# Optimization experiments

Hardware: AMD Instinct MI355X
Metric: run time of the kernel (lower is better)

## Reference

```python
import jax, jax.numpy as jnp
import numpy as np

DIM = 1024
NHEAD = 16
HEAD_DIM = DIM // NHEAD


def setup_inputs() -> dict:
    key = jax.random.key(0)
    k_x, k_wqkv, k_bqkv, k_wp, k_bp = jax.random.split(key, 5)
    scale = 1.0 / np.sqrt(DIM)
    return {
        "x": jax.random.normal(k_x, (4, 2048, DIM), dtype=jnp.float32),
        "w_qkv": jax.random.uniform(k_wqkv, (DIM, 3 * DIM), minval=-scale, maxval=scale, dtype=jnp.float32),
        "b_qkv": jax.random.uniform(k_bqkv, (3 * DIM,), minval=-scale, maxval=scale, dtype=jnp.float32),
        "w_proj": jax.random.uniform(k_wp, (DIM, DIM), minval=-scale, maxval=scale, dtype=jnp.float32),
        "b_proj": jax.random.uniform(k_bp, (DIM,), minval=-scale, maxval=scale, dtype=jnp.float32),
    }


def reference(x, w_qkv, b_qkv, w_proj, b_proj):
    B, N, D = x.shape
    # qkv projection: [B,N,3D] -> [3,B,H,N,hd]
    qkv = x @ w_qkv + b_qkv
    qkv = qkv.reshape(B, N, 3, NHEAD, HEAD_DIM).transpose(2, 0, 3, 1, 4)
    q, k, v = qkv[0], qkv[1], qkv[2]
    # naive full attention: scores [B,H,N,N]
    attn = jnp.einsum("bhqd,bhkd->bhqk", q, k) / jnp.sqrt(jnp.float32(HEAD_DIM))
    attn = jax.nn.softmax(attn, axis=-1)
    out = jnp.einsum("bhqk,bhkd->bhqd", attn, v)  # [B,H,N,hd]
    out = out.transpose(0, 2, 1, 3).reshape(B, N, D)
    return out @ w_proj + b_proj
```

## Files before the change

kernel.cpp:

```cpp
#include <hip/hip_runtime.h>
#include <math.h>

#define DIM     1024
#define NHEAD   16
#define HD      64
#define BATCH   4
#define SEQ     2048
#define MTOT    (BATCH * SEQ)
#define QKV_N   (3 * DIM)

typedef __attribute__((ext_vector_type(8))) short bf16x8;
typedef __attribute__((ext_vector_type(4))) float f32x4;
typedef unsigned int u32;
typedef unsigned short u16;

__device__ __forceinline__ u16 f2bf(float f) {
    u32 u = __float_as_uint(f);
    return (u16)((u + 0x7fffu + ((u >> 16) & 1u)) >> 16);
}

__device__ __forceinline__ float exp2_fast(float x) {
    float r; asm("v_exp_f32 %0, %1" : "=v"(r) : "v"(x)); return r;
}

__device__ __forceinline__ u32 cvtpk_bf16(float lo, float hi) {
    u32 r; asm("v_cvt_pk_bf16_f32 %0, %1, %2" : "=v"(r) : "v"(lo), "v"(hi));
    return r;
}

__device__ __forceinline__ void gload_lds16(const u16* g, u16* l) {
    __builtin_amdgcn_global_load_lds((const __attribute__((address_space(1))) u32*)g,
                                     (__attribute__((address_space(3))) u32*)l, 16, 0, 0);
}

__global__ __launch_bounds__(256) void cast_x(const float* __restrict__ in,
                                              u16* __restrict__ out) {
    const int i = (blockIdx.x * 256 + threadIdx.x) * 4;
    const float4 v = *(const float4*)&in[i];
    ushort4 o;
    o.x = f2bf(v.x); o.y = f2bf(v.y); o.z = f2bf(v.z); o.w = f2bf(v.w);
    *(ushort4*)&out[i] = o;
}

__global__ __launch_bounds__(256) void cast_transpose(const float* __restrict__ W,
                                                      u16* __restrict__ Wt,
                                                      int K, int N) {
    __shared__ float Ls[64][65];
    const int k0 = blockIdx.x * 64, n0 = blockIdx.y * 64;
    const int t = threadIdx.x;
    const int r = t >> 4, c4 = (t & 15) << 2;
    #pragma unroll
    for (int i = 0; i < 4; ++i) {
        const float4 v = *(const float4*)&W[(size_t)(k0 + r + i * 16) * N + n0 + c4];
        Ls[r + i * 16][c4 + 0] = v.x; Ls[r + i * 16][c4 + 1] = v.y;
        Ls[r + i * 16][c4 + 2] = v.z; Ls[r + i * 16][c4 + 3] = v.w;
    }
    __syncthreads();
    #pragma unroll
    for (int i = 0; i < 4; ++i) {
        const int nr = r + i * 16;
        ushort4 o;
        o.x = f2bf(Ls[c4 + 0][nr]); o.y = f2bf(Ls[c4 + 1][nr]);
        o.z = f2bf(Ls[c4 + 2][nr]); o.w = f2bf(Ls[c4 + 3][nr]);
        *(ushort4*)&Wt[(size_t)(n0 + nr) * K + k0 + c4] = o;
    }
}

#define GEMM_STAGE(buf, kof, Aptr, Bptr)                                       \
    _Pragma("unroll") for (int i = 0; i < 2; ++i) {                            \
        const int row = w * 32 + i * 16 + (lane >> 2);                         \
        const int slot = (lane & 3) ^ ((row >> 1) & 3);                        \
        gload_lds16(&Aptr[(size_t)(m0 + row) * DIM + (kof) + slot * 8],        \
                    &As[buf][(w * 32 + i * 16) * 32]);                         \
        gload_lds16(&Bptr[(size_t)(n0 + row) * DIM + (kof) + slot * 8],        \
                    &Bs[buf][(w * 32 + i * 16) * 32]);                         \
    }

#define GEMM_MAINLOOP(Aptr, Bptr)                                              \
    __shared__ __align__(16) u16 As[2][128 * 32];                              \
    __shared__ __align__(16) u16 Bs[2][128 * 32];                              \
    const int t = threadIdx.x;                                                 \
    const int lane = t & 63, w = t >> 6;                                       \
    const int n0 = blockIdx.x * 128;                                           \
    const int m0 = blockIdx.y * 128;                                           \
    const int wm = (w & 1) * 64, wn = (w >> 1) * 64;                           \
    const int g = lane >> 4, li = lane & 15;                                   \
    f32x4 acc[4][4];                                                           \
    _Pragma("unroll") for (int mt = 0; mt < 4; ++mt)                           \
        _Pragma("unroll") for (int nt = 0; nt < 4; ++nt)                       \
            acc[mt][nt] = (f32x4){0.f, 0.f, 0.f, 0.f};                         \
    GEMM_STAGE(0, 0, Aptr, Bptr)                                               \
    __syncthreads();                                                           \
    int cur = 0;                                                               \
    for (int k0 = 0; k0 < DIM; k0 += 32) {                                     \
        if (k0 + 32 < DIM) { GEMM_STAGE(cur ^ 1, k0 + 32, Aptr, Bptr) }        \
        bf16x8 a[4], b[4];                                                     \
        _Pragma("unroll") for (int mt = 0; mt < 4; ++mt) {                     \
            const int row = wm + mt * 16 + li;                                 \
            const int slot = g ^ ((row >> 1) & 3);                             \
            a[mt] = *(const bf16x8*)&As[cur][row * 32 + slot * 8];             \
        }                                                                      \
        _Pragma("unroll") for (int nt = 0; nt < 4; ++nt) {                     \
            const int row = wn + nt * 16 + li;                                 \
            const int slot = g ^ ((row >> 1) & 3);                             \
            b[nt] = *(const bf16x8*)&Bs[cur][row * 32 + slot * 8];             \
        }                                                                      \
        _Pragma("unroll") for (int mt = 0; mt < 4; ++mt)                       \
            _Pragma("unroll") for (int nt = 0; nt < 4; ++nt)                   \
                acc[mt][nt] = __builtin_amdgcn_mfma_f32_16x16x32_bf16(         \
                    a[mt], b[nt], acc[mt][nt], 0, 0, 0);                       \
        __syncthreads();                                                       \
        cur ^= 1;                                                              \
    }

#define QSCALE 0.18033688011112042f
__global__ __launch_bounds__(256) void gemm_qkv(
    const u16* __restrict__ A, const u16* __restrict__ Bt,
    const float* __restrict__ bias,
    u16* __restrict__ qo, u16* __restrict__ ko, u16* __restrict__ vo)
{
    GEMM_MAINLOOP(A, Bt)
    #pragma unroll
    for (int nt = 0; nt < 4; ++nt) {
        const int n = n0 + wn + nt * 16 + li;
        const int which = n >> 10;
        const int head  = (n >> 6) & 15;
        const int hd    = n & 63;
        const float bv = bias[n];
        if (which == 2) {
            #pragma unroll
            for (int mt = 0; mt < 4; ++mt) {
                const int m = m0 + wm + mt * 16 + g * 4;
                const int bb = m >> 11, tok = m & 2047;
                const u32 p0 = cvtpk_bf16(acc[mt][nt][0] + bv, acc[mt][nt][1] + bv);
                const u32 p1 = cvtpk_bf16(acc[mt][nt][2] + bv, acc[mt][nt][3] + bv);
                u16* d = &vo[((size_t)(bb * NHEAD + head) * HD + hd) * SEQ + tok];
                *(u32*)&d[0] = p0;
                *(u32*)&d[2] = p1;
            }
        } else {
            u16* dst = (which == 0) ? qo : ko;
            const float scale = (which == 0) ? QSCALE : 1.0f;
            #pragma unroll
            for (int mt = 0; mt < 4; ++mt) {
                #pragma unroll
                for (int r = 0; r < 4; ++r) {
                    const int m = m0 + wm + mt * 16 + g * 4 + r;
                    const int bb = m >> 11, tok = m & 2047;
                    dst[((size_t)(bb * NHEAD + head) * SEQ + tok) * HD + hd] =
                        f2bf((acc[mt][nt][r] + bv) * scale);
                }
            }
        }
    }
}

__global__ __launch_bounds__(256) void gemm_proj(
    const u16* __restrict__ A, const u16* __restrict__ Bt,
    const float* __restrict__ bias, float* __restrict__ out)
{
    GEMM_MAINLOOP(A, Bt)
    #pragma unroll
    for (int nt = 0; nt < 4; ++nt) {
        const int n = n0 + wn + nt * 16 + li;
        const float bv = bias[n];
        #pragma unroll
        for (int mt = 0; mt < 4; ++mt) {
            #pragma unroll
            for (int r = 0; r < 4; ++r) {
                const int m = m0 + wm + mt * 16 + g * 4 + r;
                out[(size_t)m * DIM + n] = acc[mt][nt][r] + bv;
            }
        }
    }
}

#define NKT  (SEQ / 64)
#define ATTN_STAGE(buf, ktile)                                                 \
    _Pragma("unroll") for (int i = 0; i < 2; ++i) {                            \
        const int rho = w * 16 + i * 8 + srow;                                 \
        const int key = (rho & 32) | (((rho >> 2) & 3) << 3)                   \
                      | (((rho >> 4) & 1) << 2) | (rho & 3);                   \
        const int sl = (sslot ^ (rho & 7)) << 3;                               \
        gload_lds16(&kg[(size_t)(ktile) * (64 * HD) + (size_t)key * HD + sl],  \
                    &Ks[buf][(w * 16 + i * 8) * 64]);                          \
        gload_lds16(&vg[(size_t)rho * SEQ + (ktile) * 64 + sl],                \
                    &Vs[buf][(w * 16 + i * 8) * 64]);                          \
    }

__global__ __launch_bounds__(256) void attn_mfma(
    const u16* __restrict__ q, const u16* __restrict__ k,
    const u16* __restrict__ v, u16* __restrict__ ao)
{
    __shared__ __align__(16) u16 Ks[3][64 * 64];
    __shared__ __align__(16) u16 Vs[3][64 * 64];

    const int t = threadIdx.x;
    const int lane = t & 63, w = t >> 6;
    const int g = lane >> 4, li = lane & 15;

    int flat = blockIdx.y * 16 + blockIdx.x;
    flat = (flat & 7) * 128 + (flat >> 3);
    const int q0 = (flat & 15) * 128;
    const int bh = flat >> 4;
    const size_t base = (size_t)bh * SEQ * HD;
    const u16* kg = k + base;
    const u16* vg = v + (size_t)bh * HD * SEQ;

    bf16x8 qf[2][2];
    #pragma unroll
    for (int h = 0; h < 2; ++h) {
        const size_t qrow = base + (size_t)(q0 + w * 32 + h * 16 + li) * HD;
        qf[h][0] = *(const bf16x8*)&q[qrow + g * 8];
        qf[h][1] = *(const bf16x8*)&q[qrow + 32 + g * 8];
    }

    float lsum[2] = {0.f, 0.f};
    f32x4 oacc[2][4];
    #pragma unroll
    for (int h = 0; h < 2; ++h)
        #pragma unroll
        for (int nt = 0; nt < 4; ++nt) oacc[h][nt] = (f32x4){0.f, 0.f, 0.f, 0.f};

    const int srow = lane >> 3;
    const int sslot = lane & 7;
    const int x8 = li & 15 & 7;

    ATTN_STAGE(0, 0)
    ATTN_STAGE(1, 1)

    int c0 = 0;
    for (int kt = 0; kt < NKT; ++kt) {
        if (kt + 1 < NKT) {
            asm volatile("s_waitcnt vmcnt(4)" ::: "memory");
        } else {
            asm volatile("s_waitcnt vmcnt(0)" ::: "memory");
        }
        __builtin_amdgcn_s_barrier();
        __builtin_amdgcn_sched_barrier(0);

        if (kt + 2 < NKT) {
            const int sslot3 = (c0 >= 1) ? c0 - 1 : c0 + 2;
            ATTN_STAGE(sslot3, kt + 2)
        }

        const u16* Kc = Ks[c0];
        const u16* Vc = Vs[c0];

        f32x4 s[2][4];
        #pragma unroll
        for (int nt = 0; nt < 4; ++nt) {
            const int rowb = (nt * 16 + li) << 6;
            const bf16x8 kf0 = *(const bf16x8*)&Kc[rowb + ((g ^ x8) << 3)];
            const bf16x8 kf1 = *(const bf16x8*)&Kc[rowb + (((g ^ 4) ^ x8) << 3)];
            #pragma unroll
            for (int h = 0; h < 2; ++h) {
                f32x4 c = (f32x4){0.f, 0.f, 0.f, 0.f};
                c = __builtin_amdgcn_mfma_f32_16x16x32_bf16(kf0, qf[h][0], c, 0, 0, 0);
                c = __builtin_amdgcn_mfma_f32_16x16x32_bf16(kf1, qf[h][1], c, 0, 0, 0);
                s[h][nt] = c;
            }
        }

        bf16x8 pb[2][2];
        #pragma unroll
        for (int h = 0; h < 2; ++h) {
            float rs = 0.f;
            #pragma unroll
            for (int nt = 0; nt < 4; ++nt)
                #pragma unroll
                for (int r = 0; r < 4; ++r) {
                    const float p = exp2_fast(s[h][nt][r]);
                    s[h][nt][r] = p;
                    rs += p;
                }
            lsum[h] += rs;
            #pragma unroll
            for (int ks = 0; ks < 2; ++ks) {
                union { u32 u[4]; bf16x8 v8; } uu;
                uu.u[0] = cvtpk_bf16(s[h][2 * ks][0],     s[h][2 * ks][1]);
                uu.u[1] = cvtpk_bf16(s[h][2 * ks][2],     s[h][2 * ks][3]);
                uu.u[2] = cvtpk_bf16(s[h][2 * ks + 1][0], s[h][2 * ks + 1][1]);
                uu.u[3] = cvtpk_bf16(s[h][2 * ks + 1][2], s[h][2 * ks + 1][3]);
                pb[h][ks] = uu.v8;
            }
        }

        #pragma unroll
        for (int ks = 0; ks < 2; ++ks) {
            #pragma unroll
            for (int nt = 0; nt < 4; ++nt) {
                const bf16x8 vb = *(const bf16x8*)
                    &Vc[((nt * 16 + li) << 6) + (((g ^ (ks << 2)) ^ x8) << 3)];
                #pragma unroll
                for (int h = 0; h < 2; ++h)
                    oacc[h][nt] = __builtin_amdgcn_mfma_f32_16x16x32_bf16(
                        vb, pb[h][ks], oacc[h][nt], 0, 0, 0);
            }
        }

        c0 = (c0 == 2) ? 0 : c0 + 1;
    }

    const int bb = bh >> 4, hh = bh & 15;
    #pragma unroll
    for (int h = 0; h < 2; ++h) {
        float lf = lsum[h];
        lf += __shfl_xor(lf, 16);
        lf += __shfl_xor(lf, 32);
        const float inv = 1.0f / lf;
        const int tok = q0 + w * 32 + h * 16 + li;
        u16* dst = &ao[(size_t)(bb * SEQ + tok) * DIM + hh * HD];
        #pragma unroll
        for (int nt = 0; nt < 4; ++nt) {
            const u32 p0 = cvtpk_bf16(oacc[h][nt][0] * inv, oacc[h][nt][1] * inv);
            const u32 p1 = cvtpk_bf16(oacc[h][nt][2] * inv, oacc[h][nt][3] * inv);
            *(u32*)&dst[nt * 16 + g * 4]     = p0;
            *(u32*)&dst[nt * 16 + g * 4 + 2] = p1;
        }
    }
}

extern "C" void kernel_launch(void* const* d_in, const int* in_sizes, int n_in,
                              void* d_out, int out_size, void* d_ws, size_t ws_size,
                              hipStream_t stream)
{
    const float* x      = (const float*)d_in[0];
    const float* w_qkv  = (const float*)d_in[1];
    const float* b_qkv  = (const float*)d_in[2];
    const float* w_proj = (const float*)d_in[3];
    const float* b_proj = (const float*)d_in[4];
    float* out = (float*)d_out;

    u16* xb  = (u16*)d_ws;
    u16* wqt = xb  + (size_t)MTOT * DIM;
    u16* wpt = wqt + (size_t)QKV_N * DIM;
    u16* qb  = wpt + (size_t)DIM * DIM;
    u16* kb  = qb  + (size_t)MTOT * DIM;
    u16* vb  = kb  + (size_t)MTOT * DIM;
    u16* aob = vb  + (size_t)MTOT * DIM;

    cast_x<<<(MTOT * DIM) / 1024, 256, 0, stream>>>(x, xb);
    cast_transpose<<<dim3(DIM / 64, QKV_N / 64), 256, 0, stream>>>(w_qkv, wqt, DIM, QKV_N);
    cast_transpose<<<dim3(DIM / 64, DIM / 64), 256, 0, stream>>>(w_proj, wpt, DIM, DIM);

    gemm_qkv<<<dim3(QKV_N / 128, MTOT / 128), 256, 0, stream>>>(xb, wqt, b_qkv, qb, kb, vb);
    attn_mfma<<<dim3(SEQ / 128, BATCH * NHEAD), 256, 0, stream>>>(qb, kb, vb, aob);
    gemm_proj<<<dim3(DIM / 128, MTOT / 128), 256, 0, stream>>>(aob, wpt, b_proj, out);
}
```

Measured before the change: 210.3 us.

## Split attention warps across key halves and reduce partial outputs via LDS

Changes the per-warp work split in the attention kernel. Each warp now owns 64 query rows and half of each 64-key tile (2x2 warp grid) instead of 32 query rows over the full key tile. Each warp reuses its K fragments across 4 query subtiles, and V/P MFMAs drop to one k-step per tile. Partial O accumulators and row sums from the two key-half warps are combined through LDS at the end. The cost is more accumulator registers (16 f32x4 versus 8), possibly lower occupancy, and an extra LDS reduction with two block barriers.

```diff
diff --git a/kernel.cpp b/kernel.cpp
--- a/kernel.cpp
+++ b/kernel.cpp
@@ -198,6 +198,7 @@
     const int t = threadIdx.x;
     const int lane = t & 63, w = t >> 6;
     const int g = lane >> 4, li = lane & 15;
+    const int qw = w & 1, kw = w >> 1;
 
     int flat = blockIdx.y * 16 + blockIdx.x;
     flat = (flat & 7) * 128 + (flat >> 3);
@@ -207,24 +208,24 @@
     const u16* kg = k + base;
     const u16* vg = v + (size_t)bh * HD * SEQ;
 
-    bf16x8 qf[2][2];
-    #pragma unroll
-    for (int h = 0; h < 2; ++h) {
-        const size_t qrow = base + (size_t)(q0 + w * 32 + h * 16 + li) * HD;
+    bf16x8 qf[4][2];
+    #pragma unroll
+    for (int h = 0; h < 4; ++h) {
+        const size_t qrow = base + (size_t)(q0 + qw * 64 + h * 16 + li) * HD;
         qf[h][0] = *(const bf16x8*)&q[qrow + g * 8];
         qf[h][1] = *(const bf16x8*)&q[qrow + 32 + g * 8];
     }
 
-    float lsum[2] = {0.f, 0.f};
-    f32x4 oacc[2][4];
-    #pragma unroll
-    for (int h = 0; h < 2; ++h)
+    float lsum[4] = {0.f, 0.f, 0.f, 0.f};
+    f32x4 oacc[4][4];
+    #pragma unroll
+    for (int h = 0; h < 4; ++h)
         #pragma unroll
         for (int nt = 0; nt < 4; ++nt) oacc[h][nt] = (f32x4){0.f, 0.f, 0.f, 0.f};
 
     const int srow = lane >> 3;
     const int sslot = lane & 7;
-    const int x8 = li & 15 & 7;
+    const int x8 = li & 7;
 
     ATTN_STAGE(0, 0)
     ATTN_STAGE(1, 1)
@@ -240,83 +241,103 @@
         __builtin_amdgcn_sched_barrier(0);
 
         if (kt + 2 < NKT) {
-            const int sslot3 = (c0 >= 1) ? c0 - 1 : c0 + 2;
-            ATTN_STAGE(sslot3, kt + 2)
+            const int st3 = (c0 >= 1) ? c0 - 1 : c0 + 2;
+            ATTN_STAGE(st3, kt + 2)
         }
 
         const u16* Kc = Ks[c0];
         const u16* Vc = Vs[c0];
 
-        f32x4 s[2][4];
-        #pragma unroll
-        for (int nt = 0; nt < 4; ++nt) {
-            const int rowb = (nt * 16 + li) << 6;
-            const bf16x8 kf0 = *(const bf16x8*)&Kc[rowb + ((g ^ x8) << 3)];
-            const bf16x8 kf1 = *(const bf16x8*)&Kc[rowb + (((g ^ 4) ^ x8) << 3)];
-            #pragma unroll
-            for (int h = 0; h < 2; ++h) {
+        bf16x8 kf[2][2];
+        #pragma unroll
+        for (int ntl = 0; ntl < 2; ++ntl) {
+            const int rowb = ((kw * 2 + ntl) * 16 + li) << 6;
+            kf[ntl][0] = *(const bf16x8*)&Kc[rowb + ((g ^ x8) << 3)];
+            kf[ntl][1] = *(const bf16x8*)&Kc[rowb + (((g ^ 4) ^ x8) << 3)];
+        }
+
+        bf16x8 pb[4];
+        #pragma unroll
+        for (int h = 0; h < 4; ++h) {
+            f32x4 s[2];
+            #pragma unroll
+            for (int ntl = 0; ntl < 2; ++ntl) {
                 f32x4 c = (f32x4){0.f, 0.f, 0.f, 0.f};
-                c = __builtin_amdgcn_mfma_f32_16x16x32_bf16(kf0, qf[h][0], c, 0, 0, 0);
-                c = __builtin_amdgcn_mfma_f32_16x16x32_bf16(kf1, qf[h][1], c, 0, 0, 0);
-                s[h][nt] = c;
-            }
-        }
-
-        bf16x8 pb[2][2];
-        #pragma unroll
-        for (int h = 0; h < 2; ++h) {
+                c = __builtin_amdgcn_mfma_f32_16x16x32_bf16(kf[ntl][0], qf[h][0], c, 0, 0, 0);
+                c = __builtin_amdgcn_mfma_f32_16x16x32_bf16(kf[ntl][1], qf[h][1], c, 0, 0, 0);
+                s[ntl] = c;
+            }
             float rs = 0.f;
             #pragma unroll
-            for (int nt = 0; nt < 4; ++nt)
+            for (int ntl = 0; ntl < 2; ++ntl)
                 #pragma unroll
                 for (int r = 0; r < 4; ++r) {
-                    const float p = exp2_fast(s[h][nt][r]);
-                    s[h][nt][r] = p;
+                    const float p = exp2_fast(s[ntl][r]);
+                    s[ntl] [r] = p;
                     rs += p;
                 }
             lsum[h] += rs;
-            #pragma unroll
-            for (int ks = 0; ks < 2; ++ks) {
-                union { u32 u[4]; bf16x8 v8; } uu;
-                uu.u[0] = cvtpk_bf16(s[h][2 * ks][0],     s[h][2 * ks][1]);
-                uu.u[1] = cvtpk_bf16(s[h][2 * ks][2],     s[h][2 * ks][3]);
-                uu.u[2] = cvtpk_bf16(s[h][2 * ks + 1][0], s[h][2 * ks + 1][1]);
-                uu.u[3] = cvtpk_bf16(s[h][2 * ks + 1][2], s[h][2 * ks + 1][3]);
-                pb[h][ks] = uu.v8;
-            }
-        }
-
-        #pragma unroll
-        for (int ks = 0; ks < 2; ++ks) {
+            union { u32 u[4]; bf16x8 v8; } uu;
+            uu.u[0] = cvtpk_bf16(s[0][0], s[0][1]);
+            uu.u[1] = cvtpk_bf16(s[0][2], s[0][3]);
+            uu.u[2] = cvtpk_bf16(s[1][0], s[1][1]);
+            uu.u[3] = cvtpk_bf16(s[1][2], s[1][3]);
+            pb[h] = uu.v8;
+        }
+
+        #pragma unroll
+        for (int nt = 0; nt < 4; ++nt) {
+            const bf16x8 vb = *(const bf16x8*)
+                &Vc[((nt * 16 + li) << 6) + (((g ^ (kw << 2)) ^ x8) << 3)];
+            #pragma unroll
+            for (int h = 0; h < 4; ++h)
+                oacc[h][nt] = __builtin_amdgcn_mfma_f32_16x16x32_bf16(
+                    vb, pb[h], oacc[h][nt], 0, 0, 0);
+        }
+
+        c0 = (c0 == 2) ? 0 : c0 + 1;
+    }
+
+    float lf[4];
+    #pragma unroll
+    for (int h = 0; h < 4; ++h) {
+        float v0 = lsum[h];
+        v0 += __shfl_xor(v0, 16);
+        v0 += __shfl_xor(v0, 32);
+        lf[h] = v0;
+    }
+
+    __syncthreads();
+    float* sc = (kw == 0) ? (float*)&Ks[0][0] : (float*)&Vs[0][0];
+    if (kw == 1) {
+        float* mysc = (qw == 0) ? (float*)&Ks[0][0] : (float*)&Vs[0][0];
+        #pragma unroll
+        for (int h = 0; h < 4; ++h) {
+            #pragma unroll
+            for (int nt = 0; nt < 4; ++nt)
+                *(f32x4*)&mysc[((h * 4 + nt) * 64 + lane) * 4] = oacc[h][nt];
+            mysc[4096 + h * 64 + lane] = lf[h];
+        }
+    }
+    __syncthreads();
+    if (kw == 0) {
+        float* psc = (qw == 0) ? (float*)&Ks[0][0] : (float*)&Vs[0][0];
+        const int bb = bh >> 4, hh = bh & 15;
+        #pragma unroll
+        for (int h = 0; h < 4; ++h) {
+            const float inv = 1.0f / (lf[h] + psc[4096 + h * 64 + lane]);
+            const int tok = q0 + qw * 64 + h * 16 + li;
+            u16* dst = &ao[(size_t)(bb * SEQ + tok) * DIM + hh * HD];
             #pragma unroll
             for (int nt = 0; nt < 4; ++nt) {
-                const bf16x8 vb = *(const bf16x8*)
-                    &Vc[((nt * 16 + li) << 6) + (((g ^ (ks << 2)) ^ x8) << 3)];
-                #pragma unroll
-                for (int h = 0; h < 2; ++h)
-                    oacc[h][nt] = __builtin_amdgcn_mfma_f32_16x16x32_bf16(
-                        vb, pb[h][ks], oacc[h][nt], 0, 0, 0);
-            }
-        }
-
-        c0 = (c0 == 2) ? 0 : c0 + 1;
-    }
-
-    const int bb = bh >> 4, hh = bh & 15;
-    #pragma unroll
-    for (int h = 0; h < 2; ++h) {
-        float lf = lsum[h];
-        lf += __shfl_xor(lf, 16);
-        lf += __shfl_xor(lf, 32);
-        const float inv = 1.0f / lf;
-        const int tok = q0 + w * 32 + h * 16 + li;
-        u16* dst = &ao[(size_t)(bb * SEQ + tok) * DIM + hh * HD];
-        #pragma unroll
-        for (int nt = 0; nt < 4; ++nt) {
-            const u32 p0 = cvtpk_bf16(oacc[h][nt][0] * inv, oacc[h][nt][1] * inv);
-            const u32 p1 = cvtpk_bf16(oacc[h][nt][2] * inv, oacc[h][nt][3] * inv);
-            *(u32*)&dst[nt * 16 + g * 4]     = p0;
-            *(u32*)&dst[nt * 16 + g * 4 + 2] = p1;
+                const f32x4 po = *(const f32x4*)&psc[((h * 4 + nt) * 64 + lane) * 4];
+                const u32 p0 = cvtpk_bf16((oacc[h][nt][0] + po[0]) * inv,
+                                          (oacc[h][nt][1] + po[1]) * inv);
+                const u32 p1 = cvtpk_bf16((oacc[h][nt][2] + po[2]) * inv,
+                                          (oacc[h][nt][3] + po[3]) * inv);
+                *(u32*)&dst[nt * 16 + g * 4]     = p0;
+                *(u32*)&dst[nt * 16 + g * 4 + 2] = p1;
+            }
         }
     }
 }
```

Measured after the change: 223.3 us. 1.06x slower.
